# Kernel tuning notes

Measured on AMD Instinct MI355X. Metric: run time of the kernel, lower is better.

## Reference

```python
import jax, jax.numpy as jnp
import numpy as np

N, E, G = 50000, 150000, 200
D, ED_IN, EH = 320, 15, 32
NB, NT = 3, 9  # conv blocks, edge types


def setup_inputs() -> dict:
    key = jax.random.key(0)
    ks = jax.random.split(key, 16)
    s = 0.02
    return {
        "x": jax.random.normal(ks[0], (N, D), jnp.float32),
        "batch": jnp.sort(jax.random.randint(ks[1], (N,), 0, G)),
        "edge_indices": jax.random.randint(ks[2], (NT, 2, E), 0, N),
        "edge_attrs": jax.random.normal(ks[3], (NT, E, ED_IN), jnp.float32),
        "W1": jax.random.normal(ks[4], (2 * D + ED_IN, EH), jnp.float32) * s,
        "b1": jnp.zeros((EH,), jnp.float32),
        "W2": jax.random.normal(ks[5], (EH, EH), jnp.float32) * s,
        "b2": jnp.zeros((EH,), jnp.float32),
        "Wq": jax.random.normal(ks[6], (NB, NT, D, D), jnp.float32) * s,
        "bq": jnp.zeros((NB, NT, D), jnp.float32),
        "Wk": jax.random.normal(ks[7], (NB, NT, D, D), jnp.float32) * s,
        "bk": jnp.zeros((NB, NT, D), jnp.float32),
        "Wv": jax.random.normal(ks[8], (NB, NT, D, D), jnp.float32) * s,
        "bv": jnp.zeros((NB, NT, D), jnp.float32),
        "We": jax.random.normal(ks[9], (NB, NT, EH, D), jnp.float32) * s,
        "be": jnp.zeros((NB, NT, D), jnp.float32),
        "Ws": jax.random.normal(ks[10], (NB, NT, D, D), jnp.float32) * s,
        "bs": jnp.zeros((NB, NT, D), jnp.float32),
        "gamma": jnp.ones((NB, D), jnp.float32),
        "beta": jnp.zeros((NB, D), jnp.float32),
    }


def _transformer_conv(x, src, dst, ea, Wq, bq, Wk, bk, Wv, bv, We, be, Ws, bs):
    # PyG TransformerConv, heads=1, edge_dim=EH, eval mode (no dropout).
    q = (x @ Wq + bq)[dst]                    # [E, D] query at destination
    e = ea @ We + be                          # [E, D] projected edge attr
    k = (x @ Wk + bk)[src] + e                # [E, D]
    v = (x @ Wv + bv)[src] + e                # [E, D]
    alpha = (q * k).sum(-1) / jnp.sqrt(jnp.float32(D))  # [E]
    amax = jax.ops.segment_max(alpha, dst, num_segments=N)
    amax = jnp.where(jnp.isfinite(amax), amax, 0.0)     # guard empty segments
    ex = jnp.exp(alpha - amax[dst])
    denom = jax.ops.segment_sum(ex, dst, num_segments=N)
    w = ex / (denom[dst] + 1e-16)
    out = jax.ops.segment_sum(w[:, None] * v, dst, num_segments=N)
    return out + x @ Ws + bs                  # root/skip connection


def _graph_layer_norm(x, batch, gamma, beta):
    # PyG gnn.norm.LayerNorm, mode='graph': normalize per graph over nodes+channels.
    cnt = jax.ops.segment_sum(jnp.ones((N,), x.dtype), batch, num_segments=G)
    norm = jnp.maximum(cnt, 1.0) * D          # elements per graph
    mean = jax.ops.segment_sum(x.sum(-1), batch, num_segments=G) / norm
    xc = x - mean[batch][:, None]
    var = jax.ops.segment_sum((xc * xc).sum(-1), batch, num_segments=G) / norm
    out = xc / jnp.sqrt(var + 1e-5)[batch][:, None]
    return out * gamma + beta


def reference(x, batch, edge_indices, edge_attrs, W1, b1, W2, b2,
              Wq, bq, Wk, bk, Wv, bv, We, be, Ws, bs, gamma, beta):
    # Edge MLP preprocessing (uses original node features x).
    new_ea = []
    for t in range(NT):
        src, dst = edge_indices[t, 0], edge_indices[t, 1]
        cat = jnp.concatenate([x[src], x[dst], edge_attrs[t]], axis=-1)  # [E, 655]
        h = jax.nn.leaky_relu(cat @ W1 + b1)
        new_ea.append(h @ W2 + b2)

    h = x
    for b in range(NB):
        acc = jnp.zeros_like(h)
        for t in range(NT):
            src, dst = edge_indices[t, 0], edge_indices[t, 1]
            acc = acc + _transformer_conv(
                h, src, dst, new_ea[t],
                Wq[b, t], bq[b, t], Wk[b, t], bk[b, t], Wv[b, t], bv[b, t],
                We[b, t], be[b, t], Ws[b, t], bs[b, t])
        x_ = jax.nn.leaky_relu(acc / 9.0)
        x_ = _graph_layer_norm(x_, batch, gamma[b], beta[b])
        h = 0.5 * (h + x_)

    return jax.ops.segment_max(h, batch, num_segments=G)  # global max pool [G, D]
```

## Files before the change

### kernel.cpp

```cpp
#include <hip/hip_runtime.h>

#define N_NODES 50000
#define N_EDGE  150000
#define N_GRAPH 200
#define DIM     320
#define EDI     15
#define EH      32
#define NBLK    3
#define NTYP    9
#define NPAD    51200
#define BPT     50
#define QLD     1000

typedef unsigned short u16;
typedef unsigned int   u32;
typedef __bf16 bf16x8 __attribute__((ext_vector_type(8)));
typedef float  f32x4  __attribute__((ext_vector_type(4)));

__device__ __forceinline__ float b2f(u16 s) {
    u32 u = ((u32)s) << 16;
    return __builtin_bit_cast(float, u);
}
__device__ __forceinline__ float b2f_lo(u32 u) { return __builtin_bit_cast(float, u << 16); }
__device__ __forceinline__ float b2f_hi(u32 u) { return __builtin_bit_cast(float, u & 0xffff0000u); }
__device__ __forceinline__ u16 f2b(float f) {
    u32 u = __builtin_bit_cast(u32, f);
    u = (u + 0x7fffu + ((u >> 16) & 1u)) >> 16;
    return (u16)u;
}

__device__ __forceinline__ void gll16(const u16* g, u32 ldsAddr) {
    u32 m0v = (u32)__builtin_amdgcn_readfirstlane((int)ldsAddr);
    asm volatile("s_mov_b32 m0, %0\n\t"
                 "global_load_lds_dwordx4 %1, off"
                 :: "s"(m0v), "v"((unsigned long long)(size_t)g)
                 : "memory");
}

__global__ __launch_bounds__(256) void gemm_kernel(
    const u16* __restrict__ A, int Mstride,
    const u16* __restrict__ Bst, const float* __restrict__ bias,
    u16* __restrict__ Cb, float* __restrict__ Cf,
    int ldc, int out_cols, int M, int NP, int KQ, int mode)
{
    const int tid = threadIdx.x;
    const int wave = tid >> 6, lane = tid & 63;
    const int n0 = blockIdx.x * 128, m0 = blockIdx.y * 128;
    const int wm = (wave & 1) << 6, wn = (wave >> 1) << 6;
    const int lm = lane & 15, quad = lane >> 4;

    __shared__ uint4 smem[2][2][512];
    const u32 ldsBase = (u32)(size_t)&smem[0][0][0];

    f32x4 acc[4][4] = {};
    const int nIter = KQ >> 2;

    auto stage = [&](int s, int buf) {
        const int c0 = s << 2;
        const u32 bufBase = ldsBase + (u32)buf * 16384u;
#pragma unroll
        for (int u = 0; u < 2; ++u) {
            const int i = wave + (u << 2);
            const int chunk = i >> 1, half = (i & 1) << 6;
            const u16* ga = A + ((size_t)(c0 + chunk) * Mstride + m0 + half + lane) * 8;
            gll16(ga, bufBase + (u32)i * 1024u);
            const u16* gb = Bst + ((size_t)(c0 + chunk) * NP + n0 + half + lane) * 8;
            gll16(gb, bufBase + 8192u + (u32)i * 1024u);
        }
    };

    stage(0, 0);
    asm volatile("s_waitcnt vmcnt(0)" ::: "memory");
    __syncthreads();

    int cur = 0;
    for (int s = 0; s < nIter; ++s) {
        if (s + 1 < nIter) stage(s + 1, cur ^ 1);
        const uint4* aT = &smem[cur][0][0];
        const uint4* bT = &smem[cur][1][0];
        bf16x8 af[4], bfr[4];
#pragma unroll
        for (int mi = 0; mi < 4; ++mi)
            af[mi] = __builtin_bit_cast(bf16x8, aT[quad * 128 + wm + mi * 16 + lm]);
#pragma unroll
        for (int ni = 0; ni < 4; ++ni)
            bfr[ni] = __builtin_bit_cast(bf16x8, bT[quad * 128 + wn + ni * 16 + lm]);
#pragma unroll
        for (int mi = 0; mi < 4; ++mi)
#pragma unroll
            for (int ni = 0; ni < 4; ++ni)
                acc[mi][ni] = __builtin_amdgcn_mfma_f32_16x16x32_bf16(af[mi], bfr[ni], acc[mi][ni], 0, 0, 0);
        asm volatile("s_waitcnt vmcnt(0)" ::: "memory");
        __syncthreads();
        cur ^= 1;
    }

#pragma unroll
    for (int mi = 0; mi < 4; ++mi) {
        int row = m0 + wm + mi * 16 + quad * 4;
#pragma unroll
        for (int ni = 0; ni < 4; ++ni) {
            int col = n0 + wn + ni * 16 + lm;
            float bv = bias ? bias[col] : 0.f;
#pragma unroll
            for (int r = 0; r < 4; ++r) {
                int rr = row + r;
                if (rr < M && col < out_cols) {
                    float v = acc[mi][ni][r] + bv;
                    size_t off = (size_t)rr * ldc + col;
                    if (mode == 0)      Cb[off] = f2b(v);
                    else if (mode == 1) Cf[off] = v;
                    else                Cf[off] += v;
                }
            }
        }
    }
}

__global__ void k_convert_x(const float* __restrict__ x, u16* __restrict__ hb) {
    int i = blockIdx.x * 256 + threadIdx.x;
    if (i >= N_NODES * DIM) return;
    int node = i / DIM, c = i - node * DIM;
    hb[((size_t)(c >> 3) * N_NODES + node) * 8 + (c & 7)] = f2b(x[i]);
}

__global__ void k_prep_qkvW(const float* __restrict__ Wq, const float* __restrict__ Wk,
                            const float* __restrict__ Wv, u16* __restrict__ Bst) {
    int i = blockIdx.x * 256 + threadIdx.x;
    if (i >= 27 * 40 * 1024) return;
    int col = i & 1023, kq = (i >> 10) % 40, bt = i / (40 * 1024);
    if (col >= 960 && col < 993) return;
    u16 tmp[8];
    if (col >= 993) {
#pragma unroll
        for (int r = 0; r < 8; ++r) tmp[r] = 0;
    } else {
        const float* W; int c;
        if (col < 320)      { W = Wq; c = col; }
        else if (col < 640) { W = Wk; c = col - 320; }
        else                { W = Wv; c = col - 640; }
#pragma unroll
        for (int r = 0; r < 8; ++r)
            tmp[r] = f2b(W[((size_t)bt * 320 + kq * 8 + r) * 320 + c]);
    }
    *(uint4*)(&Bst[(((size_t)bt * 40 + kq) * 1024 + col) * 8]) = *(uint4*)tmp;
}

__global__ __launch_bounds__(256) void k_prep_ext(
    const float* __restrict__ Wq, const float* __restrict__ bq,
    const float* __restrict__ We, const float* __restrict__ be,
    u16* __restrict__ Bst, float* __restrict__ biasQkv)
{
    __shared__ float WeL[33 * 321];
    int bt = blockIdx.x, kt = blockIdx.y;
    for (int i = threadIdx.x; i < 33 * 320; i += 256) {
        int r = i / 320, d = i - r * 320;
        WeL[r * 321 + d] = (r < 32) ? We[((size_t)bt * 32 + r) * 320 + d]
                                    : be[(size_t)bt * 320 + d];
    }
    __syncthreads();
    if (kt < 10) {
        int k  = kt * 32 + (threadIdx.x >> 3);
        int ct = threadIdx.x & 7;
        const float* wq = Wq + ((size_t)bt * 320 + k) * 320;
        float dot[5] = {0.f, 0.f, 0.f, 0.f, 0.f};
        for (int d = 0; d < 320; ++d) {
            float w = wq[d];
            dot[0] += w * WeL[ct * 321 + d];
            dot[1] += w * WeL[(ct + 8) * 321 + d];
            dot[2] += w * WeL[(ct + 16) * 321 + d];
            dot[3] += w * WeL[(ct + 24) * 321 + d];
            dot[4] += w * WeL[32 * 321 + d];
        }
#pragma unroll
        for (int u = 0; u < 4; ++u)
            Bst[(((size_t)bt * 40 + (k >> 3)) * 1024 + 960 + ct + u * 8) * 8 + (k & 7)] = f2b(dot[u]);
        if (ct == 0)
            Bst[(((size_t)bt * 40 + (k >> 3)) * 1024 + 992) * 8 + (k & 7)] = f2b(dot[4]);
    } else {
        int c = threadIdx.x;
        if (c < 33) {
            const float* b = bq + (size_t)bt * 320;
            float s = 0.f;
            for (int d = 0; d < 320; ++d) s += b[d] * WeL[c * 321 + d];
            biasQkv[bt * 1024 + 960 + c] = s;
        }
    }
}

__global__ void k_prep_qkvB(const float* __restrict__ bq, const float* __restrict__ bk,
                            const float* __restrict__ bv, float* __restrict__ bias) {
    int i = blockIdx.x * 256 + threadIdx.x;
    if (i >= 27 * 1024) return;
    int col = i & 1023, bt = i >> 10;
    float v;
    if (col < 320)       v = bq[bt * 320 + col];
    else if (col < 640)  v = bk[bt * 320 + col - 320];
    else if (col < 960)  v = bv[bt * 320 + col - 640];
    else if (col >= 993) v = 0.f;
    else return;
    bias[i] = v;
}

__global__ void k_prep_skipW(const float* __restrict__ Ws, u16* __restrict__ Bst) {
    int i = blockIdx.x * 256 + threadIdx.x;
    if (i >= 3 * 320 * 384) return;
    int col = i % 384, k = (i / 384) % 320, b = i / (384 * 320);
    float v = 0.f;
    if (col < 320)
        for (int t = 0; t < 9; ++t)
            v += Ws[((size_t)(b * 9 + t) * 320 + k) * 320 + col];
    Bst[(((size_t)b * 40 + (k >> 3)) * 384 + col) * 8 + (k & 7)] = f2b(v);
}
__global__ void k_prep_skipB(const float* __restrict__ bs, float* __restrict__ bias) {
    int i = blockIdx.x * 256 + threadIdx.x;
    if (i >= 3 * 384) return;
    int col = i % 384, b = i / 384;
    float v = 0.f;
    if (col < 320)
        for (int t = 0; t < 9; ++t) v += bs[(b * 9 + t) * 320 + col];
    bias[i] = v;
}

__global__ void k_prep_sWe(const float* __restrict__ We, const float* __restrict__ be,
                           u16* __restrict__ Bst) {
    int i = blockIdx.x * 256 + threadIdx.x;
    if (i >= 3 * 40 * 384) return;
    int col = i % 384, kq = (i / 384) % 40, b = i / (384 * 40);
    u16 tmp[8];
#pragma unroll
    for (int r = 0; r < 8; ++r) {
        int k = kq * 8 + r;
        float v = 0.f;
        if (col < 320 && k < 306) {
            int t = k / 34, j = k - t * 34;
            int bt = b * 9 + t;
            if (j < 32)       v = We[((size_t)bt * 32 + j) * 320 + col];
            else if (j == 32) v = be[(size_t)bt * 320 + col];
        }
        tmp[r] = f2b(v);
    }
    *(uint4*)(&Bst[(((size_t)b * 40 + kq) * 384 + col) * 8]) = *(uint4*)tmp;
}

__global__ void k_prep_w1W(const float* __restrict__ W1, u16* __restrict__ Bst) {
    int i = blockIdx.x * 256 + threadIdx.x;
    if (i >= 320 * 128) return;
    int col = i & 127, k = i >> 7;
    float v = 0.f;
    if (col < 32)      v = W1[(size_t)k * 32 + col];
    else if (col < 64) v = W1[(size_t)(320 + k) * 32 + (col - 32)];
    Bst[((size_t)(k >> 3) * 128 + col) * 8 + (k & 7)] = f2b(v);
}

__global__ void k_csr_zero(int* __restrict__ cnt) {
    int i = blockIdx.x * 256 + threadIdx.x;
    if (i < NTYP * NPAD) cnt[i] = 0;
}
__global__ void k_csr_count(const int* __restrict__ eidx, int* __restrict__ cnt) {
    int i = blockIdx.x * 256 + threadIdx.x;
    if (i >= NTYP * N_EDGE) return;
    int t = i / N_EDGE, e = i - t * N_EDGE;
    int dst = eidx[(size_t)(t * 2 + 1) * N_EDGE + e];
    atomicAdd(&cnt[t * NPAD + dst], 1);
}
__global__ __launch_bounds__(1024) void k_csr_scan1(const int* __restrict__ cnt,
                                                    int* __restrict__ rowStart,
                                                    int* __restrict__ blockSum) {
    __shared__ int tmp[1024];
    int t = blockIdx.y, blk = blockIdx.x, tid = threadIdx.x;
    int idx = t * NPAD + blk * 1024 + tid;
    int v = cnt[idx];
    tmp[tid] = v;
    __syncthreads();
    for (int off = 1; off < 1024; off <<= 1) {
        int x = (tid >= off) ? tmp[tid - off] : 0;
        __syncthreads();
        tmp[tid] += x;
        __syncthreads();
    }
    rowStart[idx] = tmp[tid] - v;
    if (tid == 1023) blockSum[t * 64 + blk] = tmp[tid];
}
__global__ void k_csr_scan2(int* __restrict__ blockSum) {
    int t = threadIdx.x;
    if (t >= NTYP) return;
    int run = 0;
    for (int b = 0; b < BPT; ++b) {
        int v = blockSum[t * 64 + b];
        blockSum[t * 64 + b] = run;
        run += v;
    }
}
__global__ void k_csr_scan3(int* __restrict__ rowStart, const int* __restrict__ blockSum,
                            int* __restrict__ cursor) {
    int i = blockIdx.x * 256 + threadIdx.x;
    if (i >= NTYP * NPAD) return;
    int t = i / NPAD, n = i - t * NPAD;
    int v = rowStart[i] + blockSum[t * 64 + (n >> 10)];
    rowStart[i] = v;
    cursor[i] = v;
}
__global__ void k_csr_scatter(const int* __restrict__ eidx, int* __restrict__ cursor,
                              u16* __restrict__ sSrc, int* __restrict__ sEid) {
    int i = blockIdx.x * 256 + threadIdx.x;
    if (i >= NTYP * N_EDGE) return;
    int t = i / N_EDGE, e = i - t * N_EDGE;
    int src = eidx[(size_t)(t * 2) * N_EDGE + e];
    int dst = eidx[(size_t)(t * 2 + 1) * N_EDGE + e];
    int pos = atomicAdd(&cursor[t * NPAD + dst], 1);
    sSrc[(size_t)t * N_EDGE + pos] = (u16)src;
    sEid[(size_t)t * N_EDGE + pos] = e;
}

__global__ __launch_bounds__(256) void k_edge_mlp(
    const u16* __restrict__ Anodes, const int* __restrict__ eidx,
    const float* __restrict__ eattr, const float* __restrict__ W1,
    const float* __restrict__ b1, const float* __restrict__ W2,
    const float* __restrict__ b2, u16* __restrict__ outEa, int t)
{
    __shared__ float w1c[EDI][EH];
    __shared__ float w2s[EH][EH];
    __shared__ float b1s[EH], b2s[EH];
    int tid = threadIdx.x;
    for (int i = tid; i < EDI * EH; i += 256) w1c[i / EH][i % EH] = W1[(640 + i / EH) * EH + (i % EH)];
    for (int i = tid; i < EH * EH; i += 256) w2s[i / EH][i % EH] = W2[i];
    if (tid < EH) { b1s[tid] = b1[tid]; b2s[tid] = b2[tid]; }
    __syncthreads();

    int e = blockIdx.x * 256 + tid;
    if (e >= N_EDGE) return;
    int src = eidx[(size_t)(t * 2) * N_EDGE + e];
    int dst = eidx[(size_t)(t * 2 + 1) * N_EDGE + e];
    const float* eat = eattr + ((size_t)t * N_EDGE + e) * EDI;
    const u16* a1 = Anodes + (size_t)src * 64;
    const u16* a2 = Anodes + (size_t)dst * 64 + 32;

    float h1[EH];
#pragma unroll
    for (int j = 0; j < EH; ++j) h1[j] = b2f(a1[j]) + b2f(a2[j]) + b1s[j];
    for (int i = 0; i < EDI; ++i) {
        float v = eat[i];
#pragma unroll
        for (int j = 0; j < EH; ++j) h1[j] += v * w1c[i][j];
    }
#pragma unroll
    for (int j = 0; j < EH; ++j) h1[j] = h1[j] > 0.f ? h1[j] : 0.01f * h1[j];

    u16* orow = outEa + (size_t)e * EH;
    for (int j = 0; j < EH; ++j) {
        float o = b2s[j];
#pragma unroll
        for (int i = 0; i < EH; ++i) o += h1[i] * w2s[i][j];
        orow[j] = f2b(o);
    }
}

__global__ __launch_bounds__(256) void k_attn(
    const u16* __restrict__ qkv, const int* __restrict__ rowStart,
    const u16* __restrict__ sSrc, const int* __restrict__ sEid,
    const u16* __restrict__ ea, float* __restrict__ acc,
    u16* __restrict__ sST, int t34)
{
    int wave = threadIdx.x >> 6, lane = threadIdx.x & 63;
    int n = blockIdx.x * 4 + wave;
    if (n >= N_NODES) return;
    int eb = rowStart[n], ee = rowStart[n + 1];
    if (eb == ee) return;

    const u16* qrow = qkv + (size_t)n * QLD;
    uint2 qv = *(const uint2*)(qrow + 4 * lane);
    float q40 = b2f_lo(qv.x), q41 = b2f_hi(qv.x);
    float q42 = b2f_lo(qv.y), q43 = b2f_hi(qv.y);
    float q1 = b2f(qrow[256 + lane]);
    float qwl = (lane < 33) ? b2f(qrow[960 + lane]) : 0.f;
    float qwbe = __shfl(qwl, 32, 64);
    float qw = (lane < 32) ? qwl : 0.f;
    const float RS = 0.05590169943749474f;

    float m = -INFINITY, l = 0.f, as = 0.f;
    float av0 = 0.f, av1 = 0.f, av2 = 0.f, av3 = 0.f, avt = 0.f;

    int ei = eb;
    for (; ei + 2 <= ee; ei += 2) {
        int s0 = sSrc[ei], s1 = sSrc[ei + 1];
        int id0 = sEid[ei], id1 = sEid[ei + 1];
        const u16* kr0 = qkv + (size_t)s0 * QLD + 320;
        const u16* kr1 = qkv + (size_t)s1 * QLD + 320;
        uint2 k0v = *(const uint2*)(kr0 + 4 * lane);
        uint2 k1v = *(const uint2*)(kr1 + 4 * lane);
        float k0t = b2f(kr0[256 + lane]);
        float k1t = b2f(kr1[256 + lane]);
        float ea0 = (lane < 32) ? b2f(ea[(size_t)id0 * 32 + lane]) : 0.f;
        float ea1 = (lane < 32) ? b2f(ea[(size_t)id1 * 32 + lane]) : 0.f;
        float d0 = qw * ea0 + q1 * k0t
                 + q40 * b2f_lo(k0v.x) + q41 * b2f_hi(k0v.x)
                 + q42 * b2f_lo(k0v.y) + q43 * b2f_hi(k0v.y);
        float d1 = qw * ea1 + q1 * k1t
                 + q40 * b2f_lo(k1v.x) + q41 * b2f_hi(k1v.x)
                 + q42 * b2f_lo(k1v.y) + q43 * b2f_hi(k1v.y);
#pragma unroll
        for (int off = 32; off > 0; off >>= 1) {
            d0 += __shfl_xor(d0, off, 64);
            d1 += __shfl_xor(d1, off, 64);
        }
        float a0 = (d0 + qwbe) * RS, a1 = (d1 + qwbe) * RS;
        float mn = fmaxf(m, fmaxf(a0, a1));
        float sc = __expf(m - mn);
        float p0 = __expf(a0 - mn), p1 = __expf(a1 - mn);
        l = l * sc + p0 + p1;
        const u16* vr0 = kr0 + 320;
        const u16* vr1 = kr1 + 320;
        uint2 v0v = *(const uint2*)(vr0 + 4 * lane);
        uint2 v1v = *(const uint2*)(vr1 + 4 * lane);
        float v0t = b2f(vr0[256 + lane]), v1t = b2f(vr1[256 + lane]);
        av0 = av0 * sc + p0 * b2f_lo(v0v.x) + p1 * b2f_lo(v1v.x);
        av1 = av1 * sc + p0 * b2f_hi(v0v.x) + p1 * b2f_hi(v1v.x);
        av2 = av2 * sc + p0 * b2f_lo(v0v.y) + p1 * b2f_lo(v1v.y);
        av3 = av3 * sc + p0 * b2f_hi(v0v.y) + p1 * b2f_hi(v1v.y);
        avt = avt * sc + p0 * v0t + p1 * v1t;
        as = as * sc + p0 * ea0 + p1 * ea1;
        m = mn;
    }
    if (ei < ee) {
        int s0 = sSrc[ei];
        int id0 = sEid[ei];
        const u16* kr0 = qkv + (size_t)s0 * QLD + 320;
        uint2 k0v = *(const uint2*)(kr0 + 4 * lane);
        float k0t = b2f(kr0[256 + lane]);
        float ea0 = (lane < 32) ? b2f(ea[(size_t)id0 * 32 + lane]) : 0.f;
        float d0 = qw * ea0 + q1 * k0t
                 + q40 * b2f_lo(k0v.x) + q41 * b2f_hi(k0v.x)
                 + q42 * b2f_lo(k0v.y) + q43 * b2f_hi(k0v.y);
#pragma unroll
        for (int off = 32; off > 0; off >>= 1) d0 += __shfl_xor(d0, off, 64);
        float a0 = (d0 + qwbe) * RS;
        float mn = fmaxf(m, a0);
        float sc = __expf(m - mn), p0 = __expf(a0 - mn);
        l = l * sc + p0;
        const u16* vr0 = kr0 + 320;
        uint2 v0v = *(const uint2*)(vr0 + 4 * lane);
        float v0t = b2f(vr0[256 + lane]);
        av0 = av0 * sc + p0 * b2f_lo(v0v.x);
        av1 = av1 * sc + p0 * b2f_hi(v0v.x);
        av2 = av2 * sc + p0 * b2f_lo(v0v.y);
        av3 = av3 * sc + p0 * b2f_hi(v0v.y);
        avt = avt * sc + p0 * v0t;
        as = as * sc + p0 * ea0;
    }

    float inv = 1.f / l;
    float* arow = acc + (size_t)n * DIM;
    f32x4 pa = *(const f32x4*)(arow + 4 * lane);
    pa[0] += av0 * inv; pa[1] += av1 * inv;
    pa[2] += av2 * inv; pa[3] += av3 * inv;
    *(f32x4*)(arow + 4 * lane) = pa;
    arow[256 + lane] += avt * inv;
    if (lane < 33) {
        int k = t34 + lane;
        float sv = (lane < 32) ? as * inv : 1.f;
        sST[((size_t)(k >> 3) * N_NODES + n) * 8 + (k & 7)] = f2b(sv);
    }
}

__device__ __forceinline__ int lowerb(const int* a, int n, int v) {
    int lo = 0, hi = n;
    while (lo < hi) { int mid = (lo + hi) >> 1; if (a[mid] < v) lo = mid + 1; else hi = mid; }
    return lo;
}

__global__ __launch_bounds__(1024) void k_post(
    const float* __restrict__ acc, u16* __restrict__ hb,
    const int* __restrict__ batch, const float* __restrict__ gamma,
    const float* __restrict__ beta)
{
    int g = blockIdx.x;
    int start = lowerb(batch, N_NODES, g);
    int end   = lowerb(batch, N_NODES, g + 1);
    int cnt = end - start;
    if (cnt == 0) return;
    int i0 = start * DIM, i1 = end * DIM;

    float s = 0.f, ss = 0.f;
    for (int i = i0 + threadIdx.x; i < i1; i += 1024) {
        float v = acc[i] * (1.f / 9.f);
        v = v > 0.f ? v : 0.01f * v;
        s += v; ss += v * v;
    }
    __shared__ float rs[16], rss[16];
#pragma unroll
    for (int off = 32; off > 0; off >>= 1) { s += __shfl_xor(s, off, 64); ss += __shfl_xor(ss, off, 64); }
    int wave = threadIdx.x >> 6, lane = threadIdx.x & 63;
    if (lane == 0) { rs[wave] = s; rss[wave] = ss; }
    __syncthreads();
    if (threadIdx.x == 0) {
        float S = 0.f, SS = 0.f;
        for (int w = 0; w < 16; ++w) { S += rs[w]; SS += rss[w]; }
        float norm = (float)cnt * DIM;
        float mean = S / norm;
        float var = SS / norm - mean * mean;
        rs[0] = mean;
        rss[0] = rsqrtf(var + 1e-5f);
    }
    __syncthreads();
    float mean = rs[0], rsig = rss[0];
    for (int i = i0 + threadIdx.x; i < i1; i += 1024) {
        float v = acc[i] * (1.f / 9.f);
        v = v > 0.f ? v : 0.01f * v;
        int node = i / DIM, c = i - node * DIM;
        float o = (v - mean) * rsig * gamma[c] + beta[c];
        size_t hidx = ((size_t)(c >> 3) * N_NODES + node) * 8 + (c & 7);
        hb[hidx] = f2b(0.5f * (b2f(hb[hidx]) + o));
    }
}

__global__ __launch_bounds__(320) void k_maxpool(
    const u16* __restrict__ hb, const int* __restrict__ batch, float* __restrict__ out)
{
    int g = blockIdx.x, c = threadIdx.x;
    int start = lowerb(batch, N_NODES, g);
    int end   = lowerb(batch, N_NODES, g + 1);
    size_t base = (size_t)(c >> 3) * N_NODES * 8 + (c & 7);
    float m = -INFINITY;
    for (int n = start; n < end; ++n) m = fmaxf(m, b2f(hb[base + (size_t)n * 8]));
    out[(size_t)g * DIM + c] = m;
}

extern "C" void kernel_launch(void* const* d_in, const int* in_sizes, int n_in,
                              void* d_out, int out_size, void* d_ws, size_t ws_size,
                              hipStream_t stream)
{
    (void)in_sizes; (void)n_in; (void)out_size;
    const float* x     = (const float*)d_in[0];
    const int*   batch = (const int*)d_in[1];
    const int*   eidx  = (const int*)d_in[2];
    const float* eattr = (const float*)d_in[3];
    const float* W1 = (const float*)d_in[4];
    const float* b1 = (const float*)d_in[5];
    const float* W2 = (const float*)d_in[6];
    const float* b2 = (const float*)d_in[7];
    const float* Wq = (const float*)d_in[8];
    const float* bq = (const float*)d_in[9];
    const float* Wk = (const float*)d_in[10];
    const float* bk = (const float*)d_in[11];
    const float* Wv = (const float*)d_in[12];
    const float* bv = (const float*)d_in[13];
    const float* We = (const float*)d_in[14];
    const float* be = (const float*)d_in[15];
    const float* Ws = (const float*)d_in[16];
    const float* bs = (const float*)d_in[17];
    const float* gamma = (const float*)d_in[18];
    const float* beta  = (const float*)d_in[19];
    float* out = (float*)d_out;

    char* base = (char*)d_ws;
    size_t off = 0;
    auto carve = [&](size_t bytes) -> char* {
        char* r = base + off;
        off += (bytes + 255) & ~(size_t)255;
        return r;
    };
    u16*   hbKq    = (u16*)  carve((size_t)40 * N_NODES * 8 * 2 + 1024);
    float* acc     = (float*)carve((size_t)N_NODES * DIM * 4);
    u16*   qkv     = (u16*)  carve((size_t)N_NODES * QLD * 2);
    u16*   sST     = (u16*)  carve((size_t)40 * N_NODES * 8 * 2 + 1024);
    u16*   Anodes  = (u16*)  carve((size_t)N_NODES * 64 * 2);
    u16*   BstQkv  = (u16*)  carve((size_t)27 * 40 * 1024 * 8 * 2);
    float* biasQkv = (float*)carve((size_t)27 * 1024 * 4);
    u16*   BstSkip = (u16*)  carve((size_t)3 * 40 * 384 * 8 * 2);
    float* biasSkip= (float*)carve((size_t)3 * 384 * 4);
    u16*   BstSWe  = (u16*)  carve((size_t)3 * 40 * 384 * 8 * 2);
    u16*   BstW1   = (u16*)  carve((size_t)40 * 128 * 8 * 2);
    int*   cnt     = (int*)  carve((size_t)NTYP * NPAD * 4);
    int*   rowStart= (int*)  carve((size_t)NTYP * NPAD * 4);
    int*   blockSum= (int*)  carve((size_t)NTYP * 64 * 4);
    u16*   sSrc    = (u16*)  carve((size_t)NTYP * N_EDGE * 2);
    int*   sEid    = (int*)  carve((size_t)NTYP * N_EDGE * 4);
    size_t fixed = off;
    size_t bigBytes   = (size_t)NTYP * N_EDGE * EH * 2;
    size_t smallBytes = (size_t)N_EDGE * EH * 2;
    int bigEa = (ws_size >= fixed + bigBytes + (1u << 20)) ? 1 : 0;
    u16* newEa = (u16*)carve(bigEa ? bigBytes : smallBytes);

    k_convert_x<<<(N_NODES * DIM + 255) / 256, 256, 0, stream>>>(x, hbKq);
    k_prep_qkvW<<<(27 * 40 * 1024 + 255) / 256, 256, 0, stream>>>(Wq, Wk, Wv, BstQkv);
    k_prep_ext<<<dim3(27, 11), 256, 0, stream>>>(Wq, bq, We, be, BstQkv, biasQkv);
    k_prep_qkvB<<<(27 * 1024 + 255) / 256, 256, 0, stream>>>(bq, bk, bv, biasQkv);
    k_prep_skipW<<<(3 * 320 * 384 + 255) / 256, 256, 0, stream>>>(Ws, BstSkip);
    k_prep_skipB<<<(3 * 384 + 255) / 256, 256, 0, stream>>>(bs, biasSkip);
    k_prep_sWe<<<(3 * 40 * 384 + 255) / 256, 256, 0, stream>>>(We, be, BstSWe);
    k_prep_w1W<<<(320 * 128 + 255) / 256, 256, 0, stream>>>(W1, BstW1);

    k_csr_zero<<<(NTYP * NPAD + 255) / 256, 256, 0, stream>>>(cnt);
    k_csr_count<<<(NTYP * N_EDGE + 255) / 256, 256, 0, stream>>>(eidx, cnt);
    k_csr_scan1<<<dim3(BPT, NTYP), 1024, 0, stream>>>(cnt, rowStart, blockSum);
    k_csr_scan2<<<1, 64, 0, stream>>>(blockSum);
    k_csr_scan3<<<(NTYP * NPAD + 255) / 256, 256, 0, stream>>>(rowStart, blockSum, cnt);
    k_csr_scatter<<<(NTYP * N_EDGE + 255) / 256, 256, 0, stream>>>(eidx, cnt, sSrc, sEid);

    const int mt = (N_NODES + 127) / 128;
    const int et = (N_EDGE + 255) / 256;
    gemm_kernel<<<dim3(1, mt), 256, 0, stream>>>(hbKq, N_NODES, BstW1, nullptr,
                                                 Anodes, nullptr, 64, 64, N_NODES, 128, 40, 0);
    if (bigEa) {
        for (int t = 0; t < NTYP; ++t)
            k_edge_mlp<<<dim3(et), 256, 0, stream>>>(
                Anodes, eidx, eattr, W1, b1, W2, b2, newEa + (size_t)t * N_EDGE * EH, t);
    }

    for (int b = 0; b < NBLK; ++b) {
        gemm_kernel<<<dim3(3, mt), 256, 0, stream>>>(
            hbKq, N_NODES, BstSkip + (size_t)b * 40 * 384 * 8, biasSkip + b * 384,
            nullptr, acc, DIM, DIM, N_NODES, 384, 40, 1);
        hipMemsetAsync(sST, 0, (size_t)40 * N_NODES * 8 * 2, stream);
        for (int t = 0; t < NTYP; ++t) {
            int bt = b * NTYP + t;
            u16* eaT = bigEa ? (newEa + (size_t)t * N_EDGE * EH) : newEa;
            if (!bigEa)
                k_edge_mlp<<<dim3(et), 256, 0, stream>>>(
                    Anodes, eidx, eattr, W1, b1, W2, b2, eaT, t);
            gemm_kernel<<<dim3(8, mt), 256, 0, stream>>>(
                hbKq, N_NODES, BstQkv + (size_t)bt * 40 * 1024 * 8, biasQkv + bt * 1024,
                qkv, nullptr, QLD, 993, N_NODES, 1024, 40, 0);
            k_attn<<<dim3((N_NODES + 3) / 4), 256, 0, stream>>>(
                qkv, rowStart + t * NPAD, sSrc + (size_t)t * N_EDGE, sEid + (size_t)t * N_EDGE,
                eaT, acc, sST, t * 34);
        }
        gemm_kernel<<<dim3(3, mt), 256, 0, stream>>>(
            sST, N_NODES, BstSWe + (size_t)b * 40 * 384 * 8, nullptr,
            nullptr, acc, DIM, DIM, N_NODES, 384, 40, 2);
        k_post<<<N_GRAPH, 1024, 0, stream>>>(acc, hbKq, batch,
                                             gamma + b * DIM, beta + b * DIM);
    }
    k_maxpool<<<N_GRAPH, 320, 0, stream>>>(hbKq, batch, out);
}
```

Before: 6.347 ms.

## Fold Wq·Wkᵀ into query projection to drop key GEMM columns

Precomputes M = Wq·Wkᵀ per block/type so the query side produces q' = h·M (plus the folded bias term), and the attention kernel dots q' directly against raw bf16 node features kept in a new row-major hNode copy. This removes the 320 key columns from the per-type QKV GEMM (1024 to 768 padded columns), which shrinks the qkv buffer and cuts GEMM work and store traffic. It also adds an XCD-aware block swizzle to the GEMM for L2 locality. The cost is a second node-major copy of h that k_post must maintain, an extra prep GEMM, and a bf16 rounding of the fused M that can shift numerics slightly.

Measured after the change: 5.768 ms. -9.1%, faster.

```diff
diff --git a/kernel.cpp b/kernel.cpp
--- a/kernel.cpp
+++ b/kernel.cpp
@@ -10,7 +10,9 @@
 #define NTYP    9
 #define NPAD    51200
 #define BPT     50
-#define QLD     1000
+#define QLD     676
+#define QCOLS   673
+#define NPQ     768
 
 typedef unsigned short u16;
 typedef unsigned int   u32;
@@ -45,7 +47,14 @@
 {
     const int tid = threadIdx.x;
     const int wave = tid >> 6, lane = tid & 63;
-    const int n0 = blockIdx.x * 128, m0 = blockIdx.y * 128;
+
+    const int nwg = gridDim.x * gridDim.y;
+    const int flat = blockIdx.y * gridDim.x + blockIdx.x;
+    const int qq = nwg >> 3, rr = nwg & 7;
+    const int xcd = flat & 7, loc = flat >> 3;
+    const int swz = (xcd < rr ? xcd * (qq + 1) : rr * (qq + 1) + (xcd - rr) * qq) + loc;
+    const int n0 = (swz % gridDim.x) * 128, m0 = (swz / gridDim.x) * 128;
+
     const int wm = (wave & 1) << 6, wn = (wave >> 1) << 6;
     const int lm = lane & 15, quad = lane >> 4;
 
@@ -104,10 +113,10 @@
             float bv = bias ? bias[col] : 0.f;
 #pragma unroll
             for (int r = 0; r < 4; ++r) {
-                int rr = row + r;
-                if (rr < M && col < out_cols) {
+                int rr2 = row + r;
+                if (rr2 < M && col < out_cols) {
                     float v = acc[mi][ni][r] + bv;
-                    size_t off = (size_t)rr * ldc + col;
+                    size_t off = (size_t)rr2 * ldc + col;
                     if (mode == 0)      Cb[off] = f2b(v);
                     else if (mode == 1) Cf[off] = v;
                     else                Cf[off] += v;
@@ -117,38 +126,63 @@
     }
 }
 
-__global__ void k_convert_x(const float* __restrict__ x, u16* __restrict__ hb) {
+__global__ void k_convert_x(const float* __restrict__ x, u16* __restrict__ hb,
+                            u16* __restrict__ hNode) {
     int i = blockIdx.x * 256 + threadIdx.x;
     if (i >= N_NODES * DIM) return;
     int node = i / DIM, c = i - node * DIM;
-    hb[((size_t)(c >> 3) * N_NODES + node) * 8 + (c & 7)] = f2b(x[i]);
-}
-
-__global__ void k_prep_qkvW(const float* __restrict__ Wq, const float* __restrict__ Wk,
-                            const float* __restrict__ Wv, u16* __restrict__ Bst) {
-    int i = blockIdx.x * 256 + threadIdx.x;
-    if (i >= 27 * 40 * 1024) return;
-    int col = i & 1023, kq = (i >> 10) % 40, bt = i / (40 * 1024);
-    if (col >= 960 && col < 993) return;
+    u16 v = f2b(x[i]);
+    hb[((size_t)(c >> 3) * N_NODES + node) * 8 + (c & 7)] = v;
+    hNode[i] = v;
+}
+
+__global__ __launch_bounds__(256) void k_prep_M(
+    const float* __restrict__ Wq, const float* __restrict__ Wk,
+    float* __restrict__ Mf)
+{
+    __shared__ float aq[16][321];
+    __shared__ float ak[16][321];
+    int bt = blockIdx.z, e0 = blockIdx.y * 16, d0 = blockIdx.x * 16;
+    const float* wq = Wq + ((size_t)bt * 320 + e0) * 320;
+    const float* wk = Wk + ((size_t)bt * 320 + d0) * 320;
+    for (int i = threadIdx.x; i < 16 * 320; i += 256) {
+        int r = i / 320, j = i - r * 320;
+        aq[r][j] = wq[(size_t)r * 320 + j];
+        ak[r][j] = wk[(size_t)r * 320 + j];
+    }
+    __syncthreads();
+    int te = threadIdx.x >> 4, td = threadIdx.x & 15;
+    float s = 0.f;
+    for (int j = 0; j < 320; ++j) s += aq[te][j] * ak[td][j];
+    Mf[((size_t)bt * 320 + e0 + te) * 320 + d0 + td] = s;
+}
+
+__global__ void k_prep_qkvW(const float* __restrict__ Mf, const float* __restrict__ Wv,
+                            u16* __restrict__ Bst) {
+    int i = blockIdx.x * 256 + threadIdx.x;
+    if (i >= 27 * 40 * NPQ) return;
+    int col = i % NPQ, kq = (i / NPQ) % 40, bt = i / (NPQ * 40);
+    if (col >= 640 && col < QCOLS) return;
     u16 tmp[8];
-    if (col >= 993) {
+    if (col >= QCOLS) {
 #pragma unroll
         for (int r = 0; r < 8; ++r) tmp[r] = 0;
+    } else if (col < 320) {
+#pragma unroll
+        for (int r = 0; r < 8; ++r)
+            tmp[r] = f2b(Mf[((size_t)bt * 320 + kq * 8 + r) * 320 + col]);
     } else {
-        const float* W; int c;
-        if (col < 320)      { W = Wq; c = col; }
-        else if (col < 640) { W = Wk; c = col - 320; }
-        else                { W = Wv; c = col - 640; }
 #pragma unroll
         for (int r = 0; r < 8; ++r)
-            tmp[r] = f2b(W[((size_t)bt * 320 + kq * 8 + r) * 320 + c]);
-    }
-    *(uint4*)(&Bst[(((size_t)bt * 40 + kq) * 1024 + col) * 8]) = *(uint4*)tmp;
+            tmp[r] = f2b(Wv[((size_t)bt * 320 + kq * 8 + r) * 320 + (col - 320)]);
+    }
+    *(uint4*)(&Bst[(((size_t)bt * 40 + kq) * NPQ + col) * 8]) = *(uint4*)tmp;
 }
 
 __global__ __launch_bounds__(256) void k_prep_ext(
     const float* __restrict__ Wq, const float* __restrict__ bq,
     const float* __restrict__ We, const float* __restrict__ be,
+    const float* __restrict__ bk,
     u16* __restrict__ Bst, float* __restrict__ biasQkv)
 {
     __shared__ float WeL[33 * 321];
@@ -156,7 +190,7 @@
     for (int i = threadIdx.x; i < 33 * 320; i += 256) {
         int r = i / 320, d = i - r * 320;
         WeL[r * 321 + d] = (r < 32) ? We[((size_t)bt * 32 + r) * 320 + d]
-                                    : be[(size_t)bt * 320 + d];
+                                    : (be[(size_t)bt * 320 + d] + bk[(size_t)bt * 320 + d]);
     }
     __syncthreads();
     if (kt < 10) {
@@ -174,32 +208,41 @@
         }
 #pragma unroll
         for (int u = 0; u < 4; ++u)
-            Bst[(((size_t)bt * 40 + (k >> 3)) * 1024 + 960 + ct + u * 8) * 8 + (k & 7)] = f2b(dot[u]);
+            Bst[(((size_t)bt * 40 + (k >> 3)) * NPQ + 640 + ct + u * 8) * 8 + (k & 7)] = f2b(dot[u]);
         if (ct == 0)
-            Bst[(((size_t)bt * 40 + (k >> 3)) * 1024 + 992) * 8 + (k & 7)] = f2b(dot[4]);
+            Bst[(((size_t)bt * 40 + (k >> 3)) * NPQ + 672) * 8 + (k & 7)] = f2b(dot[4]);
     } else {
         int c = threadIdx.x;
         if (c < 33) {
             const float* b = bq + (size_t)bt * 320;
             float s = 0.f;
             for (int d = 0; d < 320; ++d) s += b[d] * WeL[c * 321 + d];
-            biasQkv[bt * 1024 + 960 + c] = s;
-        }
-    }
-}
-
-__global__ void k_prep_qkvB(const float* __restrict__ bq, const float* __restrict__ bk,
-                            const float* __restrict__ bv, float* __restrict__ bias) {
-    int i = blockIdx.x * 256 + threadIdx.x;
-    if (i >= 27 * 1024) return;
-    int col = i & 1023, bt = i >> 10;
-    float v;
-    if (col < 320)       v = bq[bt * 320 + col];
-    else if (col < 640)  v = bk[bt * 320 + col - 320];
-    else if (col < 960)  v = bv[bt * 320 + col - 640];
-    else if (col >= 993) v = 0.f;
-    else return;
-    bias[i] = v;
+            biasQkv[bt * 1024 + 640 + c] = s;
+        }
+    }
+}
+
+__global__ __launch_bounds__(256) void k_prep_qkvB(
+    const float* __restrict__ Wk, const float* __restrict__ bq,
+    const float* __restrict__ bv, float* __restrict__ bias)
+{
+    int i = blockIdx.x * 256 + threadIdx.x;
+    if (i >= 27 * NPQ) return;
+    int col = i % NPQ, bt = i / NPQ;
+    if (col < 320) {
+        const float4* wr = (const float4*)(Wk + ((size_t)bt * 320 + col) * 320);
+        const float4* bb = (const float4*)(bq + (size_t)bt * 320);
+        float s = 0.f;
+        for (int j = 0; j < 80; ++j) {
+            float4 a = wr[j], b = bb[j];
+            s += a.x * b.x + a.y * b.y + a.z * b.z + a.w * b.w;
+        }
+        bias[bt * 1024 + col] = s;
+    } else if (col < 640) {
+        bias[bt * 1024 + col] = bv[(size_t)bt * 320 + (col - 320)];
+    } else if (col >= QCOLS) {
+        bias[bt * 1024 + col] = 0.f;
+    }
 }
 
 __global__ void k_prep_skipW(const float* __restrict__ Ws, u16* __restrict__ Bst) {
@@ -357,7 +400,8 @@
 }
 
 __global__ __launch_bounds__(256) void k_attn(
-    const u16* __restrict__ qkv, const int* __restrict__ rowStart,
+    const u16* __restrict__ qkv, const u16* __restrict__ hNode,
+    const int* __restrict__ rowStart,
     const u16* __restrict__ sSrc, const int* __restrict__ sEid,
     const u16* __restrict__ ea, float* __restrict__ acc,
     u16* __restrict__ sST, int t34)
@@ -373,7 +417,7 @@
     float q40 = b2f_lo(qv.x), q41 = b2f_hi(qv.x);
     float q42 = b2f_lo(qv.y), q43 = b2f_hi(qv.y);
     float q1 = b2f(qrow[256 + lane]);
-    float qwl = (lane < 33) ? b2f(qrow[960 + lane]) : 0.f;
+    float qwl = (lane < 33) ? b2f(qrow[640 + lane]) : 0.f;
     float qwbe = __shfl(qwl, 32, 64);
     float qw = (lane < 32) ? qwl : 0.f;
     const float RS = 0.05590169943749474f;
@@ -385,8 +429,8 @@
     for (; ei + 2 <= ee; ei += 2) {
         int s0 = sSrc[ei], s1 = sSrc[ei + 1];
         int id0 = sEid[ei], id1 = sEid[ei + 1];
-        const u16* kr0 = qkv + (size_t)s0 * QLD + 320;
-        const u16* kr1 = qkv + (size_t)s1 * QLD + 320;
+        const u16* kr0 = hNode + (size_t)s0 * DIM;
+        const u16* kr1 = hNode + (size_t)s1 * DIM;
         uint2 k0v = *(const uint2*)(kr0 + 4 * lane);
         uint2 k1v = *(const uint2*)(kr1 + 4 * lane);
         float k0t = b2f(kr0[256 + lane]);
@@ -409,8 +453,8 @@
         float sc = __expf(m - mn);
         float p0 = __expf(a0 - mn), p1 = __expf(a1 - mn);
         l = l * sc + p0 + p1;
-        const u16* vr0 = kr0 + 320;
-        const u16* vr1 = kr1 + 320;
+        const u16* vr0 = qkv + (size_t)s0 * QLD + 320;
+        const u16* vr1 = qkv + (size_t)s1 * QLD + 320;
         uint2 v0v = *(const uint2*)(vr0 + 4 * lane);
         uint2 v1v = *(const uint2*)(vr1 + 4 * lane);
         float v0t = b2f(vr0[256 + lane]), v1t = b2f(vr1[256 + lane]);
@@ -425,7 +469,7 @@
     if (ei < ee) {
         int s0 = sSrc[ei];
         int id0 = sEid[ei];
-        const u16* kr0 = qkv + (size_t)s0 * QLD + 320;
+        const u16* kr0 = hNode + (size_t)s0 * DIM;
         uint2 k0v = *(const uint2*)(kr0 + 4 * lane);
         float k0t = b2f(kr0[256 + lane]);
         float ea0 = (lane < 32) ? b2f(ea[(size_t)id0 * 32 + lane]) : 0.f;
@@ -438,7 +482,7 @@
         float mn = fmaxf(m, a0);
         float sc = __expf(m - mn), p0 = __expf(a0 - mn);
         l = l * sc + p0;
-        const u16* vr0 = kr0 + 320;
+        const u16* vr0 = qkv + (size_t)s0 * QLD + 320;
         uint2 v0v = *(const uint2*)(vr0 + 4 * lane);
         float v0t = b2f(vr0[256 + lane]);
         av0 = av0 * sc + p0 * b2f_lo(v0v.x);
@@ -470,7 +514,7 @@
 }
 
 __global__ __launch_bounds__(1024) void k_post(
-    const float* __restrict__ acc, u16* __restrict__ hb,
+    const float* __restrict__ acc, u16* __restrict__ hb, u16* __restrict__ hNode,
     const int* __restrict__ batch, const float* __restrict__ gamma,
     const float* __restrict__ beta)
 {
@@ -509,8 +553,9 @@
         v = v > 0.f ? v : 0.01f * v;
         int node = i / DIM, c = i - node * DIM;
         float o = (v - mean) * rsig * gamma[c] + beta[c];
-        size_t hidx = ((size_t)(c >> 3) * N_NODES + node) * 8 + (c & 7);
-        hb[hidx] = f2b(0.5f * (b2f(hb[hidx]) + o));
+        u16 nb = f2b(0.5f * (b2f(hNode[i]) + o));
+        hNode[i] = nb;
+        hb[((size_t)(c >> 3) * N_NODES + node) * 8 + (c & 7)] = nb;
     }
 }
 
@@ -561,11 +606,13 @@
         return r;
     };
     u16*   hbKq    = (u16*)  carve((size_t)40 * N_NODES * 8 * 2 + 1024);
+    u16*   hNode   = (u16*)  carve((size_t)N_NODES * DIM * 2);
     float* acc     = (float*)carve((size_t)N_NODES * DIM * 4);
     u16*   qkv     = (u16*)  carve((size_t)N_NODES * QLD * 2);
     u16*   sST     = (u16*)  carve((size_t)40 * N_NODES * 8 * 2 + 1024);
     u16*   Anodes  = (u16*)  carve((size_t)N_NODES * 64 * 2);
-    u16*   BstQkv  = (u16*)  carve((size_t)27 * 40 * 1024 * 8 * 2);
+    float* Mf      = (float*)carve((size_t)27 * 320 * 320 * 4);
+    u16*   BstQkv  = (u16*)  carve((size_t)27 * 40 * NPQ * 8 * 2);
     float* biasQkv = (float*)carve((size_t)27 * 1024 * 4);
     u16*   BstSkip = (u16*)  carve((size_t)3 * 40 * 384 * 8 * 2);
     float* biasSkip= (float*)carve((size_t)3 * 384 * 4);
@@ -582,10 +629,11 @@
     int bigEa = (ws_size >= fixed + bigBytes + (1u << 20)) ? 1 : 0;
     u16* newEa = (u16*)carve(bigEa ? bigBytes : smallBytes);
 
-    k_convert_x<<<(N_NODES * DIM + 255) / 256, 256, 0, stream>>>(x, hbKq);
-    k_prep_qkvW<<<(27 * 40 * 1024 + 255) / 256, 256, 0, stream>>>(Wq, Wk, Wv, BstQkv);
-    k_prep_ext<<<dim3(27, 11), 256, 0, stream>>>(Wq, bq, We, be, BstQkv, biasQkv);
-    k_prep_qkvB<<<(27 * 1024 + 255) / 256, 256, 0, stream>>>(bq, bk, bv, biasQkv);
+    k_convert_x<<<(N_NODES * DIM + 255) / 256, 256, 0, stream>>>(x, hbKq, hNode);
+    k_prep_M<<<dim3(20, 20, 27), 256, 0, stream>>>(Wq, Wk, Mf);
+    k_prep_qkvW<<<(27 * 40 * NPQ + 255) / 256, 256, 0, stream>>>(Mf, Wv, BstQkv);
+    k_prep_ext<<<dim3(27, 11), 256, 0, stream>>>(Wq, bq, We, be, bk, BstQkv, biasQkv);
+    k_prep_qkvB<<<(27 * NPQ + 255) / 256, 256, 0, stream>>>(Wk, bq, bv, biasQkv);
     k_prep_skipW<<<(3 * 320 * 384 + 255) / 256, 256, 0, stream>>>(Ws, BstSkip);
     k_prep_skipB<<<(3 * 384 + 255) / 256, 256, 0, stream>>>(bs, biasSkip);
     k_prep_sWe<<<(3 * 40 * 384 + 255) / 256, 256, 0, stream>>>(We, be, BstSWe);
@@ -619,17 +667,17 @@
             if (!bigEa)
                 k_edge_mlp<<<dim3(et), 256, 0, stream>>>(
                     Anodes, eidx, eattr, W1, b1, W2, b2, eaT, t);
-            gemm_kernel<<<dim3(8, mt), 256, 0, stream>>>(
-                hbKq, N_NODES, BstQkv + (size_t)bt * 40 * 1024 * 8, biasQkv + bt * 1024,
-                qkv, nullptr, QLD, 993, N_NODES, 1024, 40, 0);
+            gemm_kernel<<<dim3(6, mt), 256, 0, stream>>>(
+                hbKq, N_NODES, BstQkv + (size_t)bt * 40 * NPQ * 8, biasQkv + bt * 1024,
+                qkv, nullptr, QLD, QCOLS, N_NODES, NPQ, 40, 0);
             k_attn<<<dim3((N_NODES + 3) / 4), 256, 0, stream>>>(
-                qkv, rowStart + t * NPAD, sSrc + (size_t)t * N_EDGE, sEid + (size_t)t * N_EDGE,
+                qkv, hNode, rowStart + t * NPAD, sSrc + (size_t)t * N_EDGE, sEid + (size_t)t * N_EDGE,
                 eaT, acc, sST, t * 34);
         }
         gemm_kernel<<<dim3(3, mt), 256, 0, stream>>>(
             sST, N_NODES, BstSWe + (size_t)b * 40 * 384 * 8, nullptr,
             nullptr, acc, DIM, DIM, N_NODES, 384, 40, 2);
-        k_post<<<N_GRAPH, 1024, 0, stream>>>(acc, hbKq, batch,
+        k_post<<<N_GRAPH, 1024, 0, stream>>>(acc, hbKq, hNode, batch,
                                              gamma + b * DIM, beta + b * DIM);
     }
     k_maxpool<<<N_GRAPH, 320, 0, stream>>>(hbKq, batch, out);
```
